# Kernel optimization log

Hardware: AMD Instinct MI355X
Metric: run time of the kernel (lower is better)

The kernel has to match this reference:

```python
import jax, jax.numpy as jnp
import numpy as np

KH, KW = 3, 3   # pool_size
SH, SW = 2, 2   # strides


def setup_inputs() -> dict:
    key = jax.random.key(0)
    k1, k2 = jax.random.split(key)
    inputs = jax.random.normal(k1, (16, 224, 224, 64), dtype=jnp.float32)
    kernel = jax.random.uniform(k2, (KH * KW, 64), dtype=jnp.float32)
    # build() normalizes the initial kernel to sum to one along axis 0
    kernel = kernel / jnp.sum(kernel, axis=0, keepdims=True)
    return {"inputs": inputs, "kernel": kernel}


def _owa_pool(inputs, kernel):
    B, H, W, C = inputs.shape
    ph = -(-H // SH)  # ceil, TF SAME output size
    pw = -(-W // SW)
    pad_h = max((ph - 1) * SH + KH - H, 0)
    pad_w = max((pw - 1) * SW + KW - W, 0)
    x = jnp.pad(inputs, ((0, 0),
                         (pad_h // 2, pad_h - pad_h // 2),
                         (pad_w // 2, pad_w - pad_w // 2),
                         (0, 0)))
    # im2col via gather: rows then cols
    ri = (jnp.arange(ph) * SH)[:, None] + jnp.arange(KH)[None, :]  # [ph, KH]
    ci = (jnp.arange(pw) * SW)[:, None] + jnp.arange(KW)[None, :]  # [pw, KW]
    p = x[:, ri]            # [B, ph, KH, Wp, C]
    p = p[:, :, :, ci]      # [B, ph, KH, pw, KW, C]
    p = p.transpose(0, 1, 3, 2, 4, 5).reshape(B, ph, pw, KH * KW, C)
    # descending sort over the window elements (axis 3)
    p = -jnp.sort(-p, axis=3)
    # learned ordered-weighted average: kernel is (KH*KW, C)
    return jnp.einsum('bhwkc,kc->bhwc', p, kernel)


def reference(inputs, kernel):
    return _owa_pool(inputs, kernel)
```

## Files before the change

### kernel.cpp

```cpp
#include <hip/hip_runtime.h>


#define BB 16
#define HH 224
#define WW 224
#define CC 64
#define PH 112
#define PW 112

__device__ __forceinline__ void ce(float4& a, float4& b) {
    float4 lo, hi;
    lo.x = fminf(a.x, b.x); hi.x = fmaxf(a.x, b.x);
    lo.y = fminf(a.y, b.y); hi.y = fmaxf(a.y, b.y);
    lo.z = fminf(a.z, b.z); hi.z = fmaxf(a.z, b.z);
    lo.w = fminf(a.w, b.w); hi.w = fmaxf(a.w, b.w);
    a = lo; b = hi;
}

__global__ __launch_bounds__(256) void owa_pool_kernel(
    const float* __restrict__ in, const float* __restrict__ kw,
    float* __restrict__ out) {
    int idx = blockIdx.x * blockDim.x + threadIdx.x;
    int cg  = idx & 15;
    int pix = idx >> 4;
    int ow  = pix % PW;
    int t   = pix / PW;
    int oh  = t % PH;
    int b   = t / PH;

    int c0 = cg * 4;

    float4 wgt[9];
#pragma unroll
    for (int k = 0; k < 9; ++k)
        wgt[k] = *reinterpret_cast<const float4*>(kw + k * CC + c0);

    float4 v[9];
    int ih0 = oh * 2, iw0 = ow * 2;
#pragma unroll
    for (int kh = 0; kh < 3; ++kh) {
        int ih = ih0 + kh;
#pragma unroll
        for (int kwi = 0; kwi < 3; ++kwi) {
            int iw = iw0 + kwi;
            float4 val = make_float4(0.f, 0.f, 0.f, 0.f);
            if (ih < HH && iw < WW) {
                long off = (((long)b * HH + ih) * WW + iw) * CC + c0;
                val = *reinterpret_cast<const float4*>(in + off);
            }
            v[kh * 3 + kwi] = val;
        }
    }

    ce(v[0], v[3]); ce(v[1], v[7]); ce(v[2], v[5]); ce(v[4], v[8]);
    ce(v[0], v[7]); ce(v[2], v[4]); ce(v[3], v[8]); ce(v[5], v[6]);
    ce(v[0], v[2]); ce(v[1], v[3]); ce(v[4], v[5]); ce(v[7], v[8]);
    ce(v[1], v[4]); ce(v[3], v[6]); ce(v[5], v[7]);
    ce(v[0], v[1]); ce(v[2], v[4]); ce(v[3], v[5]); ce(v[6], v[8]);
    ce(v[2], v[3]); ce(v[4], v[5]); ce(v[6], v[7]);
    ce(v[1], v[2]); ce(v[3], v[4]); ce(v[5], v[6]);

    float4 acc = make_float4(0.f, 0.f, 0.f, 0.f);
#pragma unroll
    for (int k = 0; k < 9; ++k) {
        float4 wk = wgt[8 - k];
        acc.x += v[k].x * wk.x;
        acc.y += v[k].y * wk.y;
        acc.z += v[k].z * wk.z;
        acc.w += v[k].w * wk.w;
    }

    long oidx = (((long)b * PH + oh) * PW + ow) * CC + c0;
    *reinterpret_cast<float4*>(out + oidx) = acc;
}

extern "C" void kernel_launch(void* const* d_in, const int* in_sizes, int n_in,
                              void* d_out, int out_size, void* d_ws, size_t ws_size,
                              hipStream_t stream) {
    const float* in = (const float*)d_in[0];
    const float* kw = (const float*)d_in[1];
    float* out = (float*)d_out;

    const int total_threads = BB * PH * PW * 16;
    const int block = 256;
    const int grid = (total_threads + block - 1) / block;
    owa_pool_kernel<<<grid, block, 0, stream>>>(in, kw, out);
}
```

Baseline: 287.8 us.

## Compute two adjacent output pixels per thread, XCD-remap blocks, stage weights in LDS

Each thread now produces two horizontally adjacent outputs from a shared 3x5 input window, so it issues 15 loads where two separate pixels would need 18. Block indices are remapped so that consecutive logical blocks land on the same XCD, which is meant to improve L2 locality for the overlapping rows. The 9x64 weights are staged in shared memory instead of being loaded from global memory into registers per thread. In exchange, register pressure rises and the block count halves, which lowers the available parallelism.

```diff
diff --git a/kernel.cpp b/kernel.cpp
--- a/kernel.cpp
+++ b/kernel.cpp
@@ -7,6 +7,7 @@
 #define CC 64
 #define PH 112
 #define PW 112
+#define ROWSTRIDE (WW * CC)
 
 __device__ __forceinline__ void ce(float4& a, float4& b) {
     float4 lo, hi;
@@ -17,61 +18,113 @@
     a = lo; b = hi;
 }
 
+__device__ __forceinline__ void sort9(float4 s[9]) {
+    ce(s[0], s[3]); ce(s[1], s[7]); ce(s[2], s[5]); ce(s[4], s[8]);
+    ce(s[0], s[7]); ce(s[2], s[4]); ce(s[3], s[8]); ce(s[5], s[6]);
+    ce(s[0], s[2]); ce(s[1], s[3]); ce(s[4], s[5]); ce(s[7], s[8]);
+    ce(s[1], s[4]); ce(s[3], s[6]); ce(s[5], s[7]);
+    ce(s[0], s[1]); ce(s[2], s[4]); ce(s[3], s[5]); ce(s[6], s[8]);
+    ce(s[2], s[3]); ce(s[4], s[5]); ce(s[6], s[7]);
+    ce(s[1], s[2]); ce(s[3], s[4]); ce(s[5], s[6]);
+}
+
+__device__ __forceinline__ float4 ld4(const float* p) {
+    return *reinterpret_cast<const float4*>(p);
+}
+
+#define NBLK 6272
+#define BLK_PER_XCD (NBLK / 8)
+
 __global__ __launch_bounds__(256) void owa_pool_kernel(
     const float* __restrict__ in, const float* __restrict__ kw,
     float* __restrict__ out) {
-    int idx = blockIdx.x * blockDim.x + threadIdx.x;
-    int cg  = idx & 15;
-    int pix = idx >> 4;
-    int ow  = pix % PW;
-    int t   = pix / PW;
-    int oh  = t % PH;
-    int b   = t / PH;
+    __shared__ float ksh[9 * CC];
+    for (int i = threadIdx.x; i < 9 * CC; i += 256) ksh[i] = kw[i];
+    __syncthreads();
 
-    int c0 = cg * 4;
+    int bid = blockIdx.x;
+    int lb  = (bid & 7) * BLK_PER_XCD + (bid >> 3);
 
-    float4 wgt[9];
+    int idx  = lb * 256 + threadIdx.x;
+    int cg   = idx & 15;
+    int rest = idx >> 4;
+    int owp  = rest % (PW / 2);
+    int t    = rest / (PW / 2);
+    int oh   = t % PH;
+    int b    = t / PH;
+
+    int c0  = cg * 4;
+    int ih0 = oh * 2;
+    int iw0 = owp * 4;
+
+    const float* pr0 = in + ((long)(b * HH + ih0) * WW + iw0) * CC + c0;
+    const float* pr1 = pr0 + ROWSTRIDE;
+    const float* pr2 = pr1 + ROWSTRIDE;
+
+    bool r2ok = (ih0 + 2) < HH;
+    bool c4ok = (iw0 + 4) < WW;
+
+    const float4 Z = make_float4(0.f, 0.f, 0.f, 0.f);
+    float4 v[3][5];
 #pragma unroll
-    for (int k = 0; k < 9; ++k)
-        wgt[k] = *reinterpret_cast<const float4*>(kw + k * CC + c0);
-
-    float4 v[9];
-    int ih0 = oh * 2, iw0 = ow * 2;
+    for (int k = 0; k < 4; ++k) {
+        v[0][k] = ld4(pr0 + k * CC);
+        v[1][k] = ld4(pr1 + k * CC);
+    }
+    v[0][4] = c4ok ? ld4(pr0 + 4 * CC) : Z;
+    v[1][4] = c4ok ? ld4(pr1 + 4 * CC) : Z;
+    if (r2ok) {
 #pragma unroll
-    for (int kh = 0; kh < 3; ++kh) {
-        int ih = ih0 + kh;
+        for (int k = 0; k < 4; ++k) v[2][k] = ld4(pr2 + k * CC);
+        v[2][4] = c4ok ? ld4(pr2 + 4 * CC) : Z;
+    } else {
 #pragma unroll
-        for (int kwi = 0; kwi < 3; ++kwi) {
-            int iw = iw0 + kwi;
-            float4 val = make_float4(0.f, 0.f, 0.f, 0.f);
-            if (ih < HH && iw < WW) {
-                long off = (((long)b * HH + ih) * WW + iw) * CC + c0;
-                val = *reinterpret_cast<const float4*>(in + off);
-            }
-            v[kh * 3 + kwi] = val;
-        }
+        for (int k = 0; k < 5; ++k) v[2][k] = Z;
     }
 
-    ce(v[0], v[3]); ce(v[1], v[7]); ce(v[2], v[5]); ce(v[4], v[8]);
-    ce(v[0], v[7]); ce(v[2], v[4]); ce(v[3], v[8]); ce(v[5], v[6]);
-    ce(v[0], v[2]); ce(v[1], v[3]); ce(v[4], v[5]); ce(v[7], v[8]);
-    ce(v[1], v[4]); ce(v[3], v[6]); ce(v[5], v[7]);
-    ce(v[0], v[1]); ce(v[2], v[4]); ce(v[3], v[5]); ce(v[6], v[8]);
-    ce(v[2], v[3]); ce(v[4], v[5]); ce(v[6], v[7]);
-    ce(v[1], v[2]); ce(v[3], v[4]); ce(v[5], v[6]);
+    long obase = ((long)(b * PH + oh) * PW + owp * 2) * CC + c0;
 
-    float4 acc = make_float4(0.f, 0.f, 0.f, 0.f);
+    {
+        float4 s[9];
 #pragma unroll
-    for (int k = 0; k < 9; ++k) {
-        float4 wk = wgt[8 - k];
-        acc.x += v[k].x * wk.x;
-        acc.y += v[k].y * wk.y;
-        acc.z += v[k].z * wk.z;
-        acc.w += v[k].w * wk.w;
+        for (int r = 0; r < 3; ++r) {
+            s[r * 3 + 0] = v[r][0];
+            s[r * 3 + 1] = v[r][1];
+            s[r * 3 + 2] = v[r][2];
+        }
+        sort9(s);
+        float4 acc = Z;
+#pragma unroll
+        for (int k = 0; k < 9; ++k) {
+            float4 w = *reinterpret_cast<const float4*>(&ksh[(8 - k) * CC + c0]);
+            acc.x += s[k].x * w.x;
+            acc.y += s[k].y * w.y;
+            acc.z += s[k].z * w.z;
+            acc.w += s[k].w * w.w;
+        }
+        *reinterpret_cast<float4*>(out + obase) = acc;
     }
 
-    long oidx = (((long)b * PH + oh) * PW + ow) * CC + c0;
-    *reinterpret_cast<float4*>(out + oidx) = acc;
+    {
+        float4 s[9];
+#pragma unroll
+        for (int r = 0; r < 3; ++r) {
+            s[r * 3 + 0] = v[r][2];
+            s[r * 3 + 1] = v[r][3];
+            s[r * 3 + 2] = v[r][4];
+        }
+        sort9(s);
+        float4 acc = Z;
+#pragma unroll
+        for (int k = 0; k < 9; ++k) {
+            float4 w = *reinterpret_cast<const float4*>(&ksh[(8 - k) * CC + c0]);
+            acc.x += s[k].x * w.x;
+            acc.y += s[k].y * w.y;
+            acc.z += s[k].z * w.z;
+            acc.w += s[k].w * w.w;
+        }
+        *reinterpret_cast<float4*>(out + obase + CC) = acc;
+    }
 }
 
 extern "C" void kernel_launch(void* const* d_in, const int* in_sizes, int n_in,
@@ -81,8 +134,5 @@
     const float* kw = (const float*)d_in[1];
     float* out = (float*)d_out;
 
-    const int total_threads = BB * PH * PW * 16;
-    const int block = 256;
-    const int grid = (total_threads + block - 1) / block;
-    owa_pool_kernel<<<grid, block, 0, stream>>>(in, kw, out);
+    owa_pool_kernel<<<NBLK, 256, 0, stream>>>(in, kw, out);
 }
```

Result: no change. 289.9 us (+0.7%).
